# Performance work log

Hardware: AMD Instinct MI355X
Metric: run time of the kernel (lower is better)

## Reference

```python
import jax, jax.numpy as jnp
import numpy as np

N = 10000      # nodes
E = 320000     # edges
FIN = 512      # input feature dim
H = 2          # attention heads
D = 256        # per-head out dim
NEG_SLOPE_ATT = 0.2   # PyG GATConv attention leaky relu
NEG_SLOPE = 0.01      # F.leaky_relu default
BN_EPS = 1e-5


def setup_inputs() -> dict:
    key = jax.random.key(0)
    ks = jax.random.split(key, 24)
    s = 0.05
    inp = {
        "x": jax.random.normal(ks[0], (N, FIN), jnp.float32),
        "edge_index": jax.random.randint(ks[1], (2, E), 0, N, jnp.int64),
        # GATConv params (lin has no bias in PyG)
        "w_conv": jax.random.normal(ks[2], (FIN, H * D), jnp.float32) * s,
        "att_src": jax.random.normal(ks[3], (H, D), jnp.float32) * s,
        "att_dst": jax.random.normal(ks[4], (H, D), jnp.float32) * s,
        "b_conv": jnp.zeros((H * D,), jnp.float32),
        # densea 512->256 + BN
        "w_a": jax.random.normal(ks[5], (512, 256), jnp.float32) * s,
        "b_a": jnp.zeros((256,), jnp.float32),
        "g_a": jnp.ones((256,), jnp.float32),
        "beta_a": jnp.zeros((256,), jnp.float32),
        # dense1 256->128 + BN
        "w_1": jax.random.normal(ks[6], (256, 128), jnp.float32) * s,
        "b_1": jnp.zeros((128,), jnp.float32),
        "g_1": jnp.ones((128,), jnp.float32),
        "beta_1": jnp.zeros((128,), jnp.float32),
        # dense2 128->64 + BN
        "w_2": jax.random.normal(ks[7], (128, 64), jnp.float32) * s,
        "b_2": jnp.zeros((64,), jnp.float32),
        "g_2": jnp.ones((64,), jnp.float32),
        "beta_2": jnp.zeros((64,), jnp.float32),
        # dense3 64->3
        "w_3": jax.random.normal(ks[8], (64, 3), jnp.float32) * s,
        "b_3": jnp.zeros((3,), jnp.float32),
    }
    return inp


def _bn(x, g, b):
    # BatchNorm1d, training-mode batch statistics (biased variance)
    m = x.mean(0)
    v = x.var(0)
    return g * (x - m) * jax.lax.rsqrt(v + BN_EPS) + b


def _lrelu(x):
    return jax.nn.leaky_relu(x, NEG_SLOPE)


def reference(x, edge_index, w_conv, att_src, att_dst, b_conv,
              w_a, b_a, g_a, beta_a,
              w_1, b_1, g_1, beta_1,
              w_2, b_2, g_2, beta_2,
              w_3, b_3):
    n = x.shape[0]
    # GATConv adds self-loops by default
    loops = jnp.arange(n, dtype=edge_index.dtype)
    src = jnp.concatenate([edge_index[0], loops])
    dst = jnp.concatenate([edge_index[1], loops])

    h = (x @ w_conv).reshape(n, H, D)                   # [N,H,D]
    a_src = (h * att_src).sum(-1)                       # [N,H]
    a_dst = (h * att_dst).sum(-1)                       # [N,H]
    e = jax.nn.leaky_relu(a_src[src] + a_dst[dst], NEG_SLOPE_ATT)  # [E+N,H]
    # segment softmax over incoming edges of each destination node
    emax = jax.ops.segment_max(e, dst, num_segments=n)[dst]
    ex = jnp.exp(e - emax)
    denom = jax.ops.segment_sum(ex, dst, num_segments=n)[dst]
    alpha = ex / denom                                  # [E+N,H]
    msg = h[src] * alpha[:, :, None]                    # [E+N,H,D]
    out = jax.ops.segment_sum(msg, dst, num_segments=n).reshape(n, H * D) + b_conv

    # dropout in eval mode -> identity
    y = _lrelu(out)
    y = _lrelu(_bn(y @ w_a + b_a, g_a, beta_a))
    y = _lrelu(_bn(y @ w_1 + b_1, g_1, beta_1))
    y = _lrelu(_bn(y @ w_2 + b_2, g_2, beta_2))
    y = y @ w_3 + b_3                                   # [N,3]

    # pairwise euclidean distances via gram trick
    sq = (y * y).sum(-1)
    d2 = jnp.maximum(sq[:, None] + sq[None, :] - 2.0 * (y @ y.T), 0.0)
    d = jnp.where(d2 > 1e-12, jnp.sqrt(jnp.maximum(d2, 1e-12)), 0.0)
    return d
```

## Files before the change

### kernel.cpp

```cpp
#include <hip/hip_runtime.h>
#include <math.h>

#define NNODES 10000
#define NEDGES 320000
#define ETOT   (NEDGES + NNODES)
#define FINF   512
#define HD     512
#define MAXDEG 128

typedef __attribute__((ext_vector_type(8))) _Float16 f16x8;
typedef __attribute__((ext_vector_type(8))) ushort u16x8;
typedef __attribute__((ext_vector_type(4))) float f32x4;

__device__ __forceinline__ ushort f2h(float f) {
    return __builtin_bit_cast(ushort, (_Float16)f);
}
__device__ __forceinline__ float h2f(ushort u) {
    return (float)__builtin_bit_cast(_Float16, u);
}

#define PW1 (512 * 512)
#define PW2 (PW1 + 256 * 512)
#define PW3 (PW2 + 128 * 256)
#define PW4 (PW3 + 64 * 128)
#define ZWORDS 50896
__global__ __launch_bounds__(256) void prep_kernel(
    const float* __restrict__ wc, ushort* __restrict__ wch,
    const float* __restrict__ wa, ushort* __restrict__ wah,
    const float* __restrict__ w1, ushort* __restrict__ w1h,
    const float* __restrict__ w2, ushort* __restrict__ w2h,
    int* __restrict__ zbuf)
{
    int idx = blockIdx.x * 256 + threadIdx.x;
    if (idx >= PW4) return;
    if (idx < ZWORDS) zbuf[idx] = 0;
    float v; ushort* th; int i;
    if (idx < PW1) {
        i = idx; int n = i >> 9, k = i & 511;
        v = wc[(size_t)k * 512 + n]; th = wch;
    } else if (idx < PW2) {
        i = idx - PW1; int n = i >> 9, k = i & 511;
        v = wa[(size_t)k * 256 + n]; th = wah;
    } else if (idx < PW3) {
        i = idx - PW2; int n = i >> 8, k = i & 255;
        v = w1[(size_t)k * 128 + n]; th = w1h;
    } else {
        i = idx - PW3; int n = i >> 7, k = i & 127;
        v = w2[(size_t)k * 64 + n]; th = w2h;
    }
    th[i] = f2h(v);
}

template<int BN, int AMODE, bool ATTN, bool STATS, bool OF16>
__global__ __launch_bounds__(256) void gemm_f16(
    const void* __restrict__ Ain, const ushort* __restrict__ Bh,
    void* __restrict__ Cout, int M, int N, int K,
    const float* __restrict__ att_s, const float* __restrict__ att_d,
    float* __restrict__ a_src, float* __restrict__ a_dst,
    float* __restrict__ stats,
    const float* __restrict__ bnst, const float* __restrict__ bng,
    const float* __restrict__ bnbe)
{
    constexpr int BM = 64;
    constexpr int MR = 2, NR = BN / 32;
    __shared__ ushort sA[BM][40], sB[BN][40];
    __shared__ float bsc[256], bsh[256];
    int tid = threadIdx.x;
    int lane = tid & 63, wave = tid >> 6;
    int wr = wave >> 1, wc = wave & 1;
    int bm = blockIdx.y * BM, bn = blockIdx.x * BN;
    int mrow = lane & 15, kb = lane >> 4;

    if constexpr (AMODE == 2) {
        for (int c = tid; c < K; c += 256) {
            float m = bnst[c] * (1.f / NNODES);
            float var = bnst[K + c] * (1.f / NNODES) - m * m;
            float sc = bng[c] * rsqrtf(var + 1e-5f);
            bsc[c] = sc;
            bsh[c] = bnbe[c] - m * sc;
        }
        __syncthreads();
    }

    int ar = tid >> 2, akc = tid & 3;
    int arow = bm + ar;
    bool aval = arow < M;
    size_t aoff = (size_t)(aval ? arow : 0) * K + akc * 8;
    int br, bkc;
    if constexpr (BN == 128) { br = tid >> 1; bkc = (tid & 1) * 2; }
    else { br = tid >> 2; bkc = tid & 3; }
    size_t boff = (size_t)(bn + br) * K + bkc * 8;

    f32x4 acc[MR][NR];
    #pragma unroll
    for (int i = 0; i < MR; ++i)
        #pragma unroll
        for (int j = 0; j < NR; ++j)
            acc[i][j] = (f32x4){0.f, 0.f, 0.f, 0.f};

    for (int k0 = 0; k0 < K; k0 += 32) {
        int4 va;
        if constexpr (AMODE == 0) {
            va = aval ? *(const int4*)((const ushort*)Ain + aoff + k0) : (int4){0, 0, 0, 0};
        } else {
            u16x8 us = (u16x8)0;
            if (aval) {
                const float* ap = (const float*)Ain + aoff + k0;
                float4 f0 = *(const float4*)ap;
                float4 f1 = *(const float4*)(ap + 4);
                float vv[8] = {f0.x, f0.y, f0.z, f0.w, f1.x, f1.y, f1.z, f1.w};
                #pragma unroll
                for (int j = 0; j < 8; ++j) {
                    float v = vv[j];
                    if constexpr (AMODE == 2) {
                        int c = k0 + akc * 8 + j;
                        v = fmaf(v, bsc[c], bsh[c]);
                        v = (v > 0.f) ? v : 0.01f * v;
                    }
                    us[j] = f2h(v);
                }
            }
            va = __builtin_bit_cast(int4, us);
        }
        int4 vb0 = *(const int4*)(Bh + boff + k0);
        int4 vb1;
        if constexpr (BN == 128) vb1 = *(const int4*)(Bh + boff + k0 + 8);
        __syncthreads();
        *(int4*)&sA[ar][akc * 8] = va;
        *(int4*)&sB[br][bkc * 8] = vb0;
        if constexpr (BN == 128) *(int4*)&sB[br][(bkc + 1) * 8] = vb1;
        __syncthreads();

        f16x8 fa[MR], fb[NR];
        #pragma unroll
        for (int fi = 0; fi < MR; ++fi)
            fa[fi] = *(const f16x8*)&sA[wr * 32 + fi * 16 + mrow][kb * 8];
        #pragma unroll
        for (int fj = 0; fj < NR; ++fj)
            fb[fj] = *(const f16x8*)&sB[wc * (BN / 2) + fj * 16 + mrow][kb * 8];
        #pragma unroll
        for (int fi = 0; fi < MR; ++fi)
            #pragma unroll
            for (int fj = 0; fj < NR; ++fj)
                acc[fi][fj] = __builtin_amdgcn_mfma_f32_16x16x32_f16(fa[fi], fb[fj], acc[fi][fj], 0, 0, 0);
    }

    #pragma unroll
    for (int fi = 0; fi < MR; ++fi) {
        int crow0 = bm + wr * 32 + fi * 16 + (lane >> 4) * 4;
        #pragma unroll
        for (int fj = 0; fj < NR; ++fj) {
            int ccol = bn + wc * (BN / 2) + fj * 16 + mrow;
            #pragma unroll
            for (int r = 0; r < 4; ++r) {
                int row = crow0 + r;
                if (row < M) {
                    if constexpr (OF16)
                        ((ushort*)Cout)[(size_t)row * N + ccol] = f2h(acc[fi][fj][r]);
                    else
                        ((float*)Cout)[(size_t)row * N + ccol] = acc[fi][fj][r];
                }
            }
        }
    }

    if constexpr (ATTN) {
        int hd = bn >> 8;
        float as_v[NR], ad_v[NR];
        #pragma unroll
        for (int fj = 0; fj < NR; ++fj) {
            int c = bn + wc * (BN / 2) + fj * 16 + mrow;
            as_v[fj] = att_s[c];
            ad_v[fj] = att_d[c];
        }
        #pragma unroll
        for (int fi = 0; fi < MR; ++fi)
            #pragma unroll
            for (int r = 0; r < 4; ++r) {
                float ss = 0.f, sd = 0.f;
                #pragma unroll
                for (int fj = 0; fj < NR; ++fj) {
                    float v = acc[fi][fj][r];
                    ss = fmaf(v, as_v[fj], ss);
                    sd = fmaf(v, ad_v[fj], sd);
                }
                #pragma unroll
                for (int off = 1; off < 16; off <<= 1) {
                    ss += __shfl_xor(ss, off);
                    sd += __shfl_xor(sd, off);
                }
                if (mrow == 0) {
                    int row = bm + wr * 32 + fi * 16 + (lane >> 4) * 4 + r;
                    if (row < M) {
                        atomicAdd(&a_src[2 * row + hd], ss);
                        atomicAdd(&a_dst[2 * row + hd], sd);
                    }
                }
            }
    }

    if constexpr (STATS) {
        #pragma unroll
        for (int fj = 0; fj < NR; ++fj) {
            float s = 0.f, s2 = 0.f;
            #pragma unroll
            for (int fi = 0; fi < MR; ++fi)
                #pragma unroll
                for (int r = 0; r < 4; ++r) {
                    float v = acc[fi][fj][r];
                    s += v;
                    s2 = fmaf(v, v, s2);
                }
            s  += __shfl_xor(s, 16);  s  += __shfl_xor(s, 32);
            s2 += __shfl_xor(s2, 16); s2 += __shfl_xor(s2, 32);
            if (lane < 16) {
                int c = bn + wc * (BN / 2) + fj * 16 + lane;
                atomicAdd(&stats[c], s);
                atomicAdd(&stats[N + c], s2);
            }
        }
    }
}

__global__ __launch_bounds__(256) void scatter_kernel(const int* __restrict__ ei,
    const float* __restrict__ a_src, const float* __restrict__ a_dst,
    int* __restrict__ cnt, int* __restrict__ esrc,
    float* __restrict__ p0, float* __restrict__ p1)
{
    int e = blockIdx.x * 256 + threadIdx.x;
    if (e >= ETOT) return;
    int s, d;
    if (e < NEDGES) { s = ei[e]; d = ei[NEDGES + e]; } else { s = d = e - NEDGES; }
    int pos = atomicAdd(&cnt[d], 1);
    if (pos >= MAXDEG) return;
    int slot = d * MAXDEG + pos;
    esrc[slot] = s;
    float e0 = a_src[2 * s] + a_dst[2 * d];
    e0 = (e0 > 0.f) ? e0 : 0.2f * e0;
    float e1 = a_src[2 * s + 1] + a_dst[2 * d + 1];
    e1 = (e1 > 0.f) ? e1 : 0.2f * e1;
    p0[slot] = expf(e0);
    p1[slot] = expf(e1);
}

__global__ __launch_bounds__(128) void aggregate_kernel(const ushort* __restrict__ h,
    const int* __restrict__ cnt, const int* __restrict__ esrc,
    const float* __restrict__ p0, const float* __restrict__ p1,
    const float* __restrict__ b_conv, ushort* __restrict__ yh)
{
    int n = blockIdx.x, t = threadIdx.x;
    int len = cnt[n]; if (len > MAXDEG) len = MAXDEG;
    int base = n * MAXDEG;
    const float* pp = (t < 64) ? p0 : p1;
    float a0 = 0.f, a1 = 0.f, a2 = 0.f, a3 = 0.f;
    float den = 0.f;
    for (int k = 0; k < len; ++k) {
        int src = esrc[base + k];
        float q = pp[base + k];
        ushort4 hv = ((const ushort4*)(h + (size_t)src * HD))[t];
        a0 = fmaf(q, h2f(hv.x), a0);
        a1 = fmaf(q, h2f(hv.y), a1);
        a2 = fmaf(q, h2f(hv.z), a2);
        a3 = fmaf(q, h2f(hv.w), a3);
        den += q;
    }
    float4 bc = *(const float4*)(b_conv + t * 4);
    float inv = 1.f / den;
    float o[4] = { a0 * inv + bc.x, a1 * inv + bc.y, a2 * inv + bc.z, a3 * inv + bc.w };
    ushort4 hq;
    float v;
    v = (o[0] > 0.f) ? o[0] : 0.01f * o[0]; hq.x = f2h(v);
    v = (o[1] > 0.f) ? o[1] : 0.01f * o[1]; hq.y = f2h(v);
    v = (o[2] > 0.f) ? o[2] : 0.01f * o[2]; hq.z = f2h(v);
    v = (o[3] > 0.f) ? o[3] : 0.01f * o[3]; hq.w = f2h(v);
    ((ushort4*)(yh + (size_t)n * HD))[t] = hq;
}

__global__ __launch_bounds__(256) void bn_dense3(const float* __restrict__ z2,
    const float* __restrict__ st, const float* __restrict__ g, const float* __restrict__ beta,
    const float* __restrict__ w3, const float* __restrict__ b3, float* __restrict__ y3)
{
    __shared__ float wsm[192], msm[64], rsm[64], gsm[64], bsm[64];
    int t = threadIdx.x;
    if (t < 192) wsm[t] = w3[t];
    if (t < 64) {
        float m = st[t] * (1.f / NNODES);
        float v = st[64 + t] * (1.f / NNODES) - m * m;
        msm[t] = m; rsm[t] = rsqrtf(v + 1e-5f);
        gsm[t] = g[t]; bsm[t] = beta[t];
    }
    __syncthreads();
    int n = blockIdx.x * 256 + t;
    if (n >= NNODES) return;
    const float* zr = z2 + (size_t)n * 64;
    float o0 = b3[0], o1 = b3[1], o2 = b3[2];
    #pragma unroll
    for (int c = 0; c < 64; ++c) {
        float xv = zr[c];
        xv = gsm[c] * (xv - msm[c]) * rsm[c] + bsm[c];
        xv = (xv > 0.f) ? xv : 0.01f * xv;
        o0 = fmaf(xv, wsm[3 * c],     o0);
        o1 = fmaf(xv, wsm[3 * c + 1], o1);
        o2 = fmaf(xv, wsm[3 * c + 2], o2);
    }
    y3[3 * n] = o0; y3[3 * n + 1] = o1; y3[3 * n + 2] = o2;
}

__global__ __launch_bounds__(256) void dist_kernel(const float* __restrict__ y3, float* __restrict__ out)
{
    int j0 = (blockIdx.x * 256 + threadIdx.x) * 4;
    int i0 = blockIdx.y * 64;
    if (j0 >= NNODES) return;
    const float4* yp = (const float4*)(y3 + 3 * j0);
    float4 q0 = yp[0], q1 = yp[1], q2 = yp[2];
    float xj[4] = {q0.x, q0.w, q1.z, q2.y};
    float yj[4] = {q0.y, q1.x, q1.w, q2.z};
    float zj[4] = {q0.z, q1.y, q2.x, q2.w};
    int iend = (i0 + 64 < NNODES) ? (i0 + 64) : NNODES;
    for (int i = i0; i < iend; ++i) {
        float xi = y3[3 * i], yi = y3[3 * i + 1], zi = y3[3 * i + 2];
        f32x4 dv;
        #pragma unroll
        for (int u = 0; u < 4; ++u) {
            float dx = xi - xj[u], dy = yi - yj[u], dz = zi - zj[u];
            float d2 = fmaf(dx, dx, fmaf(dy, dy, dz * dz));
            dv[u] = (d2 > 1e-12f) ? sqrtf(d2) : 0.f;
        }
        __builtin_nontemporal_store(dv, (f32x4*)(out + (size_t)i * NNODES + j0));
    }
}

extern "C" void kernel_launch(void* const* d_in, const int* in_sizes, int n_in,
                              void* d_out, int out_size, void* d_ws, size_t ws_size,
                              hipStream_t stream)
{
    (void)in_sizes; (void)n_in; (void)out_size; (void)ws_size;
    const float* x      = (const float*)d_in[0];
    const int*   ei     = (const int*)  d_in[1];
    const float* w_conv = (const float*)d_in[2];
    const float* att_s  = (const float*)d_in[3];
    const float* att_d  = (const float*)d_in[4];
    const float* b_conv = (const float*)d_in[5];
    const float* w_a  = (const float*)d_in[6];
    const float* g_a  = (const float*)d_in[8];
    const float* be_a = (const float*)d_in[9];
    const float* w_1  = (const float*)d_in[10];
    const float* g_1  = (const float*)d_in[12];
    const float* be_1 = (const float*)d_in[13];
    const float* w_2  = (const float*)d_in[14];
    const float* g_2  = (const float*)d_in[16];
    const float* be_2 = (const float*)d_in[17];
    const float* w_3  = (const float*)d_in[18];
    const float* b_3  = (const float*)d_in[19];

    char* ws = (char*)d_ws;
    size_t off = 0;
    auto take = [&](size_t bytes) {
        char* p = ws + off;
        off = (off + bytes + 255) & ~(size_t)255;
        return p;
    };
    ushort* h   = (ushort*)take((size_t)NNODES * HD * 2);
    ushort* yh  = (ushort*)take((size_t)NNODES * HD * 2);
    float* z_a  = (float*)take((size_t)NNODES * 256 * 4);
    float* z_1  = (float*)take((size_t)NNODES * 128 * 4);
    float* z_2  = (float*)take((size_t)NNODES * 64 * 4);
    float* y3   = (float*)take((size_t)NNODES * 3 * 4);
    ushort* wch = (ushort*)take((size_t)512 * 512 * 2);
    ushort* wah = (ushort*)take((size_t)256 * 512 * 2);
    ushort* w1h = (ushort*)take((size_t)128 * 256 * 2);
    ushort* w2h = (ushort*)take((size_t)64 * 128 * 2);
    int*   esrc = (int*)  take((size_t)NNODES * MAXDEG * 4);
    float* p0   = (float*)take((size_t)NNODES * MAXDEG * 4);
    float* p1   = (float*)take((size_t)NNODES * MAXDEG * 4);
    const size_t ZB = 40000 + 2048 + 1024 + 512 + 80000 + 80000;
    char*  zblk = take(ZB);
    int*   cnt  = (int*)(zblk);
    float* stA  = (float*)(zblk + 40000);
    float* st1  = (float*)(zblk + 42048);
    float* st2  = (float*)(zblk + 43072);
    float* a_src= (float*)(zblk + 43584);
    float* a_dst= (float*)(zblk + 123584);

    dim3 b256(256), b128(128);
    const int MT = (NNODES + 63) / 64;

    prep_kernel<<<dim3((PW4 + 255) / 256), b256, 0, stream>>>(
        w_conv, wch, w_a, wah, w_1, w1h, w_2, w2h, (int*)zblk);

    gemm_f16<128, 1, true, false, true><<<dim3(HD / 128, MT), b256, 0, stream>>>(
        x, wch, h, NNODES, HD, FINF, att_s, att_d, a_src, a_dst, nullptr,
        nullptr, nullptr, nullptr);

    scatter_kernel<<<dim3((ETOT + 255) / 256), b256, 0, stream>>>(
        ei, a_src, a_dst, cnt, esrc, p0, p1);

    aggregate_kernel<<<dim3(NNODES), b128, 0, stream>>>(
        h, cnt, esrc, p0, p1, b_conv, yh);

    gemm_f16<128, 0, false, true, false><<<dim3(256 / 128, MT), b256, 0, stream>>>(
        yh, wah, z_a, NNODES, 256, 512, nullptr, nullptr, nullptr, nullptr, stA,
        nullptr, nullptr, nullptr);

    gemm_f16<64, 2, false, true, false><<<dim3(128 / 64, MT), b256, 0, stream>>>(
        z_a, w1h, z_1, NNODES, 128, 256, nullptr, nullptr, nullptr, nullptr, st1,
        stA, g_a, be_a);

    gemm_f16<64, 2, false, true, false><<<dim3(64 / 64, MT), b256, 0, stream>>>(
        z_1, w2h, z_2, NNODES, 64, 128, nullptr, nullptr, nullptr, nullptr, st2,
        st1, g_1, be_1);

    bn_dense3<<<dim3((NNODES + 255) / 256), b256, 0, stream>>>(z_2, st2, g_2, be_2, w_3, b_3, y3);

    dist_kernel<<<dim3((NNODES + 1023) / 1024, (NNODES + 63) / 64), b256, 0, stream>>>(y3, (float*)d_out);
}
```

Before: 258.7 us.

## Pre-convert x to fp16, store intermediates in fp16, unroll aggregation loop

The prep kernel now also converts the input features x to fp16, so the first GEMM reads fp16 directly instead of converting fp32 per tile. The dense-layer intermediates z_a and z_1 are stored as fp16, and a new A-mode applies BN+leaky-ReLU to fp16 inputs, halving their traffic. The aggregation loop is unrolled by two to keep more gathers in flight. In exchange, x is read and written once more in the prep pass, and the fp16 intermediates give up some precision.

```diff
diff --git a/kernel.cpp b/kernel.cpp
--- a/kernel.cpp
+++ b/kernel.cpp
@@ -19,12 +19,15 @@
     return (float)__builtin_bit_cast(_Float16, u);
 }
 
+#define XC4 (NNODES * FINF / 4)
 #define PW1 (512 * 512)
 #define PW2 (PW1 + 256 * 512)
 #define PW3 (PW2 + 128 * 256)
 #define PW4 (PW3 + 64 * 128)
+#define PTOT (XC4 + PW4)
 #define ZWORDS 50896
 __global__ __launch_bounds__(256) void prep_kernel(
+    const float* __restrict__ x, ushort* __restrict__ xh,
     const float* __restrict__ wc, ushort* __restrict__ wch,
     const float* __restrict__ wa, ushort* __restrict__ wah,
     const float* __restrict__ w1, ushort* __restrict__ w1h,
@@ -32,20 +35,28 @@
     int* __restrict__ zbuf)
 {
     int idx = blockIdx.x * 256 + threadIdx.x;
-    if (idx >= PW4) return;
+    if (idx >= PTOT) return;
     if (idx < ZWORDS) zbuf[idx] = 0;
+    if (idx < XC4) {
+        float4 v = ((const float4*)x)[idx];
+        ushort4 o;
+        o.x = f2h(v.x); o.y = f2h(v.y); o.z = f2h(v.z); o.w = f2h(v.w);
+        ((ushort4*)xh)[idx] = o;
+        return;
+    }
+    int widx = idx - XC4;
     float v; ushort* th; int i;
-    if (idx < PW1) {
-        i = idx; int n = i >> 9, k = i & 511;
+    if (widx < PW1) {
+        i = widx; int n = i >> 9, k = i & 511;
         v = wc[(size_t)k * 512 + n]; th = wch;
-    } else if (idx < PW2) {
-        i = idx - PW1; int n = i >> 9, k = i & 511;
+    } else if (widx < PW2) {
+        i = widx - PW1; int n = i >> 9, k = i & 511;
         v = wa[(size_t)k * 256 + n]; th = wah;
-    } else if (idx < PW3) {
-        i = idx - PW2; int n = i >> 8, k = i & 255;
+    } else if (widx < PW3) {
+        i = widx - PW2; int n = i >> 8, k = i & 255;
         v = w1[(size_t)k * 128 + n]; th = w1h;
     } else {
-        i = idx - PW3; int n = i >> 7, k = i & 127;
+        i = widx - PW3; int n = i >> 7, k = i & 127;
         v = w2[(size_t)k * 64 + n]; th = w2h;
     }
     th[i] = f2h(v);
@@ -71,7 +82,7 @@
     int bm = blockIdx.y * BM, bn = blockIdx.x * BN;
     int mrow = lane & 15, kb = lane >> 4;
 
-    if constexpr (AMODE == 2) {
+    if constexpr (AMODE == 2 || AMODE == 3) {
         for (int c = tid; c < K; c += 256) {
             float m = bnst[c] * (1.f / NNODES);
             float var = bnst[K + c] * (1.f / NNODES) - m * m;
@@ -102,6 +113,20 @@
         int4 va;
         if constexpr (AMODE == 0) {
             va = aval ? *(const int4*)((const ushort*)Ain + aoff + k0) : (int4){0, 0, 0, 0};
+        } else if constexpr (AMODE == 3) {
+            u16x8 us = (u16x8)0;
+            if (aval) {
+                u16x8 uin = *(const u16x8*)((const ushort*)Ain + aoff + k0);
+                #pragma unroll
+                for (int j = 0; j < 8; ++j) {
+                    float v = h2f(uin[j]);
+                    int c = k0 + akc * 8 + j;
+                    v = fmaf(v, bsc[c], bsh[c]);
+                    v = (v > 0.f) ? v : 0.01f * v;
+                    us[j] = f2h(v);
+                }
+            }
+            va = __builtin_bit_cast(int4, us);
         } else {
             u16x8 us = (u16x8)0;
             if (aval) {
@@ -112,11 +137,9 @@
                 #pragma unroll
                 for (int j = 0; j < 8; ++j) {
                     float v = vv[j];
-                    if constexpr (AMODE == 2) {
-                        int c = k0 + akc * 8 + j;
-                        v = fmaf(v, bsc[c], bsh[c]);
-                        v = (v > 0.f) ? v : 0.01f * v;
-                    }
+                    int c = k0 + akc * 8 + j;
+                    v = fmaf(v, bsc[c], bsh[c]);
+                    v = (v > 0.f) ? v : 0.01f * v;
                     us[j] = f2h(v);
                 }
             }
@@ -254,15 +277,25 @@
     const float* pp = (t < 64) ? p0 : p1;
     float a0 = 0.f, a1 = 0.f, a2 = 0.f, a3 = 0.f;
     float den = 0.f;
-    for (int k = 0; k < len; ++k) {
-        int src = esrc[base + k];
-        float q = pp[base + k];
-        ushort4 hv = ((const ushort4*)(h + (size_t)src * HD))[t];
-        a0 = fmaf(q, h2f(hv.x), a0);
-        a1 = fmaf(q, h2f(hv.y), a1);
-        a2 = fmaf(q, h2f(hv.z), a2);
-        a3 = fmaf(q, h2f(hv.w), a3);
-        den += q;
+    int k = 0;
+    for (; k + 1 < len; k += 2) {
+        int s0 = esrc[base + k], s1 = esrc[base + k + 1];
+        float q0 = pp[base + k], q1 = pp[base + k + 1];
+        ushort4 hv0 = ((const ushort4*)(h + (size_t)s0 * HD))[t];
+        ushort4 hv1 = ((const ushort4*)(h + (size_t)s1 * HD))[t];
+        a0 = fmaf(q0, h2f(hv0.x), a0); a1 = fmaf(q0, h2f(hv0.y), a1);
+        a2 = fmaf(q0, h2f(hv0.z), a2); a3 = fmaf(q0, h2f(hv0.w), a3);
+        a0 = fmaf(q1, h2f(hv1.x), a0); a1 = fmaf(q1, h2f(hv1.y), a1);
+        a2 = fmaf(q1, h2f(hv1.z), a2); a3 = fmaf(q1, h2f(hv1.w), a3);
+        den += q0 + q1;
+    }
+    if (k < len) {
+        int s0 = esrc[base + k];
+        float q0 = pp[base + k];
+        ushort4 hv0 = ((const ushort4*)(h + (size_t)s0 * HD))[t];
+        a0 = fmaf(q0, h2f(hv0.x), a0); a1 = fmaf(q0, h2f(hv0.y), a1);
+        a2 = fmaf(q0, h2f(hv0.z), a2); a3 = fmaf(q0, h2f(hv0.w), a3);
+        den += q0;
     }
     float4 bc = *(const float4*)(b_conv + t * 4);
     float inv = 1.f / den;
@@ -362,8 +395,9 @@
     };
     ushort* h   = (ushort*)take((size_t)NNODES * HD * 2);
     ushort* yh  = (ushort*)take((size_t)NNODES * HD * 2);
-    float* z_a  = (float*)take((size_t)NNODES * 256 * 4);
-    float* z_1  = (float*)take((size_t)NNODES * 128 * 4);
+    ushort* xh  = (ushort*)take((size_t)NNODES * FINF * 2);
+    ushort* z_a = (ushort*)take((size_t)NNODES * 256 * 2);
+    ushort* z_1 = (ushort*)take((size_t)NNODES * 128 * 2);
     float* z_2  = (float*)take((size_t)NNODES * 64 * 4);
     float* y3   = (float*)take((size_t)NNODES * 3 * 4);
     ushort* wch = (ushort*)take((size_t)512 * 512 * 2);
@@ -385,11 +419,11 @@
     dim3 b256(256), b128(128);
     const int MT = (NNODES + 63) / 64;
 
-    prep_kernel<<<dim3((PW4 + 255) / 256), b256, 0, stream>>>(
-        w_conv, wch, w_a, wah, w_1, w1h, w_2, w2h, (int*)zblk);
-
-    gemm_f16<128, 1, true, false, true><<<dim3(HD / 128, MT), b256, 0, stream>>>(
-        x, wch, h, NNODES, HD, FINF, att_s, att_d, a_src, a_dst, nullptr,
+    prep_kernel<<<dim3((PTOT + 255) / 256), b256, 0, stream>>>(
+        x, xh, w_conv, wch, w_a, wah, w_1, w1h, w_2, w2h, (int*)zblk);
+
+    gemm_f16<128, 0, true, false, true><<<dim3(HD / 128, MT), b256, 0, stream>>>(
+        xh, wch, h, NNODES, HD, FINF, att_s, att_d, a_src, a_dst, nullptr,
         nullptr, nullptr, nullptr);
 
     scatter_kernel<<<dim3((ETOT + 255) / 256), b256, 0, stream>>>(
@@ -398,15 +432,15 @@
     aggregate_kernel<<<dim3(NNODES), b128, 0, stream>>>(
         h, cnt, esrc, p0, p1, b_conv, yh);
 
-    gemm_f16<128, 0, false, true, false><<<dim3(256 / 128, MT), b256, 0, stream>>>(
+    gemm_f16<128, 0, false, true, true><<<dim3(256 / 128, MT), b256, 0, stream>>>(
         yh, wah, z_a, NNODES, 256, 512, nullptr, nullptr, nullptr, nullptr, stA,
         nullptr, nullptr, nullptr);
 
-    gemm_f16<64, 2, false, true, false><<<dim3(128 / 64, MT), b256, 0, stream>>>(
+    gemm_f16<64, 3, false, true, true><<<dim3(128 / 64, MT), b256, 0, stream>>>(
         z_a, w1h, z_1, NNODES, 128, 256, nullptr, nullptr, nullptr, nullptr, st1,
         stA, g_a, be_a);
 
-    gemm_f16<64, 2, false, true, false><<<dim3(64 / 64, MT), b256, 0, stream>>>(
+    gemm_f16<64, 3, false, true, false><<<dim3(64 / 64, MT), b256, 0, stream>>>(
         z_1, w2h, z_2, NNODES, 64, 128, nullptr, nullptr, nullptr, nullptr, st2,
         st1, g_1, be_1);
 
```

New measurement: 245.1 us. -5.2%, faster.
